# Kernel optimization log

Hardware: AMD Instinct MI355X
Metric: run time of the kernel (lower is better)

The kernel has to match this reference:

```python
import jax, jax.numpy as jnp
import numpy as np

N = 50000   # nodes
D = 64      # feature_dim
E = 800000  # edges per edge set
NEG_SLOPE = 0.2  # PyG GATConv default


def gat_conv(x, edge_index, W, a_src, a_dst, bias):
    """PyG GATConv, heads=1, concat=True, add_self_loops=True.
    h = x W; e_{j->i} = leakyrelu(a_src.h_j + a_dst.h_i); segment-softmax over dst.
    """
    n = x.shape[0]
    h = x @ W                                   # [N, D]
    s = h @ a_src                               # [N] per-node src score
    d = h @ a_dst                               # [N] per-node dst score
    src, dst = edge_index[0], edge_index[1]
    e = jax.nn.leaky_relu(s[src] + d[dst], NEG_SLOPE)
    # remove_self_loops: mask any pre-existing self loops out of the softmax
    e = jnp.where(src == dst, jnp.float32(-1e9), e)
    # add_self_loops: one (i, i) edge per node
    loop = jnp.arange(n)
    src_all = jnp.concatenate([src, loop])
    dst_all = jnp.concatenate([dst, loop])
    e_all = jnp.concatenate([e, jax.nn.leaky_relu(s + d, NEG_SLOPE)])
    # numerically stable segment softmax over incoming edges of each dst node
    m = jax.ops.segment_max(e_all, dst_all, num_segments=n)
    p = jnp.exp(e_all - m[dst_all])
    denom = jax.ops.segment_sum(p, dst_all, num_segments=n)
    alpha = p / denom[dst_all]                  # [E + N]
    out = jax.ops.segment_sum(alpha[:, None] * h[src_all], dst_all, num_segments=n)
    return out + bias


def encode(x, edge_a, edge_b, W, a_src, a_dst, bias):
    # Original overwrites x_a/x_b each loop iteration, always reading the
    # original x, so only the final-layer encoder's single application survives.
    x_a = jax.nn.relu(gat_conv(x, edge_a, W, a_src, a_dst, bias))
    x_b = jax.nn.relu(gat_conv(x, edge_b, W, a_src, a_dst, bias))
    return x_a, x_b


def setup_inputs() -> dict:
    key = jax.random.key(0)
    ks = jax.random.split(key, 13)
    edges = [jax.random.randint(ks[i], (2, E), 0, N) for i in range(8)]
    x = jax.random.normal(ks[8], (N, D), dtype=jnp.float32)
    scale = np.float32(1.0 / np.sqrt(D))
    W = jax.random.normal(ks[9], (4, D, D), dtype=jnp.float32) * scale
    a_src = jax.random.normal(ks[10], (4, D), dtype=jnp.float32) * scale
    a_dst = jax.random.normal(ks[11], (4, D), dtype=jnp.float32) * scale
    bias = jnp.zeros((4, D), dtype=jnp.float32)
    return {"edge_tp_a": edges[0], "edge_tp_b": edges[1], "edge_tn_a": edges[2],
            "edge_tn_b": edges[3], "edge_dp_a": edges[4], "edge_dp_b": edges[5],
            "edge_dn_a": edges[6], "edge_dn_b": edges[7], "x": x, "W": W,
            "a_src": a_src, "a_dst": a_dst, "bias": bias}


def reference(edge_tp_a, edge_tp_b, edge_tn_a, edge_tn_b, edge_dp_a, edge_dp_b,
              edge_dn_a, edge_dn_b, x, W, a_src, a_dst, bias):
    # 4 encode calls, each with its own (fresh) GATConv parameters
    tp_a, tp_b = encode(x, edge_tp_a, edge_tp_b, W[0], a_src[0], a_dst[0], bias[0])
    tn_a, tn_b = encode(x, edge_tn_a, edge_tn_b, W[1], a_src[1], a_dst[1], bias[1])
    dp_a, dp_b = encode(x, edge_dp_a, edge_dp_b, W[2], a_src[2], a_dst[2], bias[2])
    dn_a, dn_b = encode(x, edge_dn_a, edge_dn_b, W[3], a_src[3], a_dst[3], bias[3])
    # original return order
    return (tp_a, tp_b, dp_a, dp_b, tn_a, tn_b, dn_a, dn_b)
```

## Files before the change

kernel.cpp:

```cpp
#include <hip/hip_runtime.h>
#include <hip/hip_bf16.h>

typedef unsigned int u32;
typedef unsigned short u16;
typedef __hip_bfloat16 bf16;

typedef __attribute__((ext_vector_type(8))) short short8;
typedef __attribute__((ext_vector_type(4))) float float4v;

#define CAP 5120

__device__ __forceinline__ float lrelu(float v) { return v > 0.f ? v : 0.2f * v; }

__device__ __forceinline__ u16 f2b(float f) {
  u32 x = __float_as_uint(f);
  u32 r = (x + 0x7fffu + ((x >> 16) & 1u)) >> 16;
  return (u16)r;
}
__device__ __forceinline__ float b2fbits(u16 b) {
  return __uint_as_float(((u32)b) << 16);
}
__device__ __forceinline__ float blo(u32 v) { return __uint_as_float(v << 16); }
__device__ __forceinline__ float bhi(u32 v) { return __uint_as_float(v & 0xffff0000u); }

struct EdgePtrs { const int* e[8]; };

__global__ __launch_bounds__(256) void CSGDN_32031866093637_kernel(u32* __restrict__ p,
                                                                   int count) {
  int i = blockIdx.x * 256 + threadIdx.x;
  if (i < count) p[i] = 0;
}


__device__ __forceinline__ void gemm_role(
    u32* smem, int g, const float* __restrict__ x, const float* __restrict__ W,
    const float* __restrict__ a_src, const float* __restrict__ a_dst,
    u16* __restrict__ H, float* __restrict__ sv, float* __restrict__ dv, int n) {
  const int p = g & 3;
  const int rowbase = (g >> 2) * 64;
  const int tid = threadIdx.x, lane = tid & 63, wv = tid >> 6;
  short* xl = (short*)smem;
  short* wl = xl + 64 * 72;
#pragma unroll
  for (int it = 0; it < 16; it++) {
    int idx = it * 256 + tid;
    int r = idx >> 6, c = idx & 63;
    int gr = rowbase + r; if (gr > n - 1) gr = n - 1;
    xl[r * 72 + c] = (short)f2b(x[(size_t)gr * 64 + c]);
  }
#pragma unroll
  for (int it = 0; it < 16; it++) {
    int idx = it * 256 + tid;
    int k = idx >> 6, nc = idx & 63;
    wl[nc * 72 + k] = (short)f2b(W[p * 4096 + k * 64 + nc]);
  }
  __syncthreads();

  const int q = lane >> 4, c15 = lane & 15;
  const int wrow0 = wv * 16;
  short8 af0 = *(const short8*)&xl[(wrow0 + c15) * 72 + 0 * 32 + q * 8];
  short8 af1 = *(const short8*)&xl[(wrow0 + c15) * 72 + 1 * 32 + q * 8];
  float4v acc[4];
#pragma unroll
  for (int nt = 0; nt < 4; nt++) {
    acc[nt] = (float4v){0.f, 0.f, 0.f, 0.f};
    short8 b0 = *(const short8*)&wl[(nt * 16 + c15) * 72 + 0 * 32 + q * 8];
    short8 b1 = *(const short8*)&wl[(nt * 16 + c15) * 72 + 1 * 32 + q * 8];
    acc[nt] = __builtin_amdgcn_mfma_f32_16x16x32_bf16(af0, b0, acc[nt], 0, 0, 0);
    acc[nt] = __builtin_amdgcn_mfma_f32_16x16x32_bf16(af1, b1, acc[nt], 0, 0, 0);
  }
  u16* Hb = H + (size_t)p * n * 64;
  float as4[4], ad4[4];
#pragma unroll
  for (int nt = 0; nt < 4; nt++) {
    as4[nt] = a_src[p * 64 + nt * 16 + c15];
    ad4[nt] = a_dst[p * 64 + nt * 16 + c15];
  }
#pragma unroll
  for (int r = 0; r < 4; r++) {
    int row_g = rowbase + wrow0 + q * 4 + r;
    bool ok = row_g < n;
#pragma unroll
    for (int nt = 0; nt < 4; nt++) {
      if (ok) Hb[(size_t)row_g * 64 + nt * 16 + c15] = f2b(acc[nt][r]);
    }
    float ps = 0.f, pd = 0.f;
#pragma unroll
    for (int nt = 0; nt < 4; nt++) {
      ps = fmaf(acc[nt][r], as4[nt], ps);
      pd = fmaf(acc[nt][r], ad4[nt], pd);
    }
#pragma unroll
    for (int o = 1; o < 16; o <<= 1) {
      ps += __shfl_xor(ps, o, 64);
      pd += __shfl_xor(pd, o, 64);
    }
    if (ok && c15 == 0) {
      sv[(size_t)p * n + row_g] = ps;
      dv[(size_t)p * n + row_g] = pd;
    }
  }
}

__device__ __forceinline__ void bin_role(
    u32* smem, int bf, EdgePtrs ep, u32* __restrict__ gcnt, u32* __restrict__ bbuf,
    int E, int nb) {
  int set = bf & 7, chunk = bf >> 3;
  const int* e = ep.e[set];
  u32* hist = smem;
  u32* gbase = smem + 256;
  u32* curs = smem + 512;
  u32* loffs = smem + 768;
  u32* sorted = smem + 1028;
  int tid = threadIdx.x, lane = tid & 63, wv = tid >> 6;
  hist[tid] = 0;
  curs[tid] = 0;
  __syncthreads();
  int start = chunk * 4096;
  u32 pk_r[16];
#pragma unroll
  for (int t = 0; t < 16; t++) {
    int i = start + t * 256 + tid;
    u32 pk = 0xffffffffu;
    if (i < E) {
      int s = e[i], d = e[E + i];
      if (s != d) {
        pk = ((u32)d << 16) | (u32)s;
        atomicAdd(&hist[d >> 8], 1u);
      }
    }
    pk_r[t] = pk;
  }
  __syncthreads();
  if (hist[tid] > 0) gbase[tid] = atomicAdd(&gcnt[set * nb + tid], hist[tid]);
  if (wv == 0) {
    u32 carry = 0;
    for (int base = 0; base < 256; base += 64) {
      u32 v = hist[base + lane], x = v;
#pragma unroll
      for (int o = 1; o < 64; o <<= 1) { u32 y = __shfl_up(x, o, 64); if (lane >= o) x += y; }
      loffs[base + lane] = carry + x - v;
      carry += __shfl(x, 63, 64);
    }
    if (lane == 0) loffs[256] = carry;
  }
  __syncthreads();
#pragma unroll
  for (int t = 0; t < 16; t++) {
    u32 pk = pk_r[t];
    if (pk != 0xffffffffu) {
      int b = pk >> 24;
      u32 pos = loffs[b] + atomicAdd(&curs[b], 1u);
      sorted[pos] = pk;
    }
  }
  __syncthreads();
  int cnt = (int)loffs[256];
  for (int j = tid; j < cnt; j += 256) {
    u32 pk = sorted[j];
    int b = pk >> 24;
    u32 gpos = gbase[b] + ((u32)j - loffs[b]);
    if (gpos >= CAP) gpos = CAP - 1;
    bbuf[((size_t)(set * nb + b)) * CAP + gpos] = pk;
  }
}

__global__ __launch_bounds__(256) void prep_kernel(
    EdgePtrs ep, u32* __restrict__ gcnt, u32* __restrict__ bbuf, int E, int nb,
    int nbin,
    const float* __restrict__ x, const float* __restrict__ W,
    const float* __restrict__ a_src, const float* __restrict__ a_dst,
    u16* __restrict__ H, float* __restrict__ sv, float* __restrict__ dv, int n) {
  __shared__ __align__(16) u32 smem[5248];
  int f = blockIdx.x;
  if (f < nbin) bin_role(smem, f, ep, gcnt, bbuf, E, nb);
  else gemm_role(smem, f - nbin, x, W, a_src, a_dst, H, sv, dv, n);
}

__global__ __launch_bounds__(512) void agg_kernel(
    const u32* __restrict__ gcnt, const u32* __restrict__ bbuf,
    const u16* __restrict__ H, const float* __restrict__ sv,
    const float* __restrict__ dv, const float* __restrict__ bias,
    float* __restrict__ out, int n, int nb) {
  const int omap[8] = {0, 1, 4, 5, 2, 3, 6, 7};
  int f = blockIdx.x;
  int set = f & 7, b = f >> 3, p = set >> 1;
  int tid = threadIdx.x, lane = tid & 63, wv = tid >> 6;
  int node0 = b << 8;
  int nn = min(256, n - node0);
  __shared__ u16 ss[CAP];
  __shared__ float spe[CAP];
  __shared__ u32 hist[256], offs[257], curs[256];
  __shared__ float dpw[256], spw[256];
  const float* sp = sv + (size_t)p * n;
  const float* dp = dv + (size_t)p * n;
  for (int i = tid; i < 256; i += 512) { hist[i] = 0; curs[i] = 0; }
  for (int i = tid; i < nn; i += 512) { dpw[i] = dp[node0 + i]; spw[i] = sp[node0 + i]; }
  __syncthreads();
  int cnt = (int)gcnt[set * nb + b];
  if (cnt > CAP) cnt = CAP;
  const u32* eb = bbuf + ((size_t)(set * nb + b)) * CAP;
  u32 pk_r[10];
  float pe_r[10];
#pragma unroll
  for (int t = 0; t < 10; t++) {
    int j = t * 512 + tid;
    u32 pk = 0;
    float pe = 0.f;
    if (j < cnt) {
      pk = eb[j];
      int s = pk & 0xffff, dl = (pk >> 16) & 255;
      atomicAdd(&hist[dl], 1u);
      pe = __expf(lrelu(sp[s] + dpw[dl]));
    }
    pk_r[t] = pk;
    pe_r[t] = pe;
  }
  __syncthreads();
  if (wv == 0) {
    u32 carry = 0;
    for (int base = 0; base < 256; base += 64) {
      u32 v = hist[base + lane];
      u32 x = v;
#pragma unroll
      for (int o = 1; o < 64; o <<= 1) { u32 y = __shfl_up(x, o, 64); if (lane >= o) x += y; }
      offs[base + lane] = carry + x - v;
      carry += __shfl(x, 63, 64);
    }
    if (lane == 0) offs[256] = carry;
  }
  __syncthreads();
#pragma unroll
  for (int t = 0; t < 10; t++) {
    int j = t * 512 + tid;
    if (j < cnt) {
      u32 pk = pk_r[t];
      int dl = (pk >> 16) & 255;
      u32 pos = offs[dl] + atomicAdd(&curs[dl], 1u);
      ss[pos] = (u16)(pk & 0xffff);
      spe[pos] = pe_r[t];
    }
  }
  __syncthreads();
  const u16* Hp = H + (size_t)p * n * 64;
  const int g = lane >> 3, sub = lane & 7;
  float4v bv0 = *(const float4v*)&bias[p * 64 + sub * 8];
  float4v bv1 = *(const float4v*)&bias[p * 64 + sub * 8 + 4];
  float* op = out + (size_t)omap[set] * n * 64;
  for (int r0 = 0; r0 < nn; r0 += 64) {
    int i = r0 + wv * 8 + g;
    bool valid = i < nn;
    int iv = valid ? i : 0;
    int beg = (int)offs[iv], end2 = (int)offs[iv + 1];
    int cntg = valid ? (end2 - beg) : 0;
    int node = node0 + iv;
    float pself = valid ? __expf(lrelu(spw[iv] + dpw[iv])) : 0.f;
    uint4 hs = *(const uint4*)(Hp + ((size_t)node << 6) + (sub << 3));
    float den = pself;
    float a0 = pself * blo(hs.x), a1 = pself * bhi(hs.x);
    float a2 = pself * blo(hs.y), a3 = pself * bhi(hs.y);
    float a4 = pself * blo(hs.z), a5 = pself * bhi(hs.z);
    float a6 = pself * blo(hs.w), a7 = pself * bhi(hs.w);
    int tmax = cntg;
#pragma unroll
    for (int o = 8; o < 64; o <<= 1) tmax = max(tmax, __shfl_xor(tmax, o, 64));
    for (int t = 0; t < tmax; t += 4) {
      bool c0 = t < cntg, c1 = t + 1 < cntg, c2 = t + 2 < cntg, c3 = t + 3 < cntg;
      int j0 = c0 ? beg + t : 0;
      int j1 = c1 ? beg + t + 1 : 0;
      int j2 = c2 ? beg + t + 2 : 0;
      int j3 = c3 ? beg + t + 3 : 0;
      float pe0 = c0 ? spe[j0] : 0.f;
      float pe1 = c1 ? spe[j1] : 0.f;
      float pe2 = c2 ? spe[j2] : 0.f;
      float pe3 = c3 ? spe[j3] : 0.f;
      int s0 = ss[j0], s1 = ss[j1], s2 = ss[j2], s3 = ss[j3];
      uint4 hv0 = *(const uint4*)(Hp + ((size_t)s0 << 6) + (sub << 3));
      uint4 hv1 = *(const uint4*)(Hp + ((size_t)s1 << 6) + (sub << 3));
      uint4 hv2 = *(const uint4*)(Hp + ((size_t)s2 << 6) + (sub << 3));
      uint4 hv3 = *(const uint4*)(Hp + ((size_t)s3 << 6) + (sub << 3));
      a0 = fmaf(pe0, blo(hv0.x), a0); a1 = fmaf(pe0, bhi(hv0.x), a1);
      a2 = fmaf(pe0, blo(hv0.y), a2); a3 = fmaf(pe0, bhi(hv0.y), a3);
      a4 = fmaf(pe0, blo(hv0.z), a4); a5 = fmaf(pe0, bhi(hv0.z), a5);
      a6 = fmaf(pe0, blo(hv0.w), a6); a7 = fmaf(pe0, bhi(hv0.w), a7);
      a0 = fmaf(pe1, blo(hv1.x), a0); a1 = fmaf(pe1, bhi(hv1.x), a1);
      a2 = fmaf(pe1, blo(hv1.y), a2); a3 = fmaf(pe1, bhi(hv1.y), a3);
      a4 = fmaf(pe1, blo(hv1.z), a4); a5 = fmaf(pe1, bhi(hv1.z), a5);
      a6 = fmaf(pe1, blo(hv1.w), a6); a7 = fmaf(pe1, bhi(hv1.w), a7);
      a0 = fmaf(pe2, blo(hv2.x), a0); a1 = fmaf(pe2, bhi(hv2.x), a1);
      a2 = fmaf(pe2, blo(hv2.y), a2); a3 = fmaf(pe2, bhi(hv2.y), a3);
      a4 = fmaf(pe2, blo(hv2.z), a4); a5 = fmaf(pe2, bhi(hv2.z), a5);
      a6 = fmaf(pe2, blo(hv2.w), a6); a7 = fmaf(pe2, bhi(hv2.w), a7);
      a0 = fmaf(pe3, blo(hv3.x), a0); a1 = fmaf(pe3, bhi(hv3.x), a1);
      a2 = fmaf(pe3, blo(hv3.y), a2); a3 = fmaf(pe3, bhi(hv3.y), a3);
      a4 = fmaf(pe3, blo(hv3.z), a4); a5 = fmaf(pe3, bhi(hv3.z), a5);
      a6 = fmaf(pe3, blo(hv3.w), a6); a7 = fmaf(pe3, bhi(hv3.w), a7);
      den += (pe0 + pe1) + (pe2 + pe3);
    }
    if (valid) {
      float rd = 1.f / den;
      float4v o0 = {fmaxf(fmaf(a0, rd, bv0.x), 0.f), fmaxf(fmaf(a1, rd, bv0.y), 0.f),
                    fmaxf(fmaf(a2, rd, bv0.z), 0.f), fmaxf(fmaf(a3, rd, bv0.w), 0.f)};
      float4v o1 = {fmaxf(fmaf(a4, rd, bv1.x), 0.f), fmaxf(fmaf(a5, rd, bv1.y), 0.f),
                    fmaxf(fmaf(a6, rd, bv1.z), 0.f), fmaxf(fmaf(a7, rd, bv1.w), 0.f)};
      *(float4v*)&op[((size_t)node << 6) + (sub << 3)] = o0;
      *(float4v*)&op[((size_t)node << 6) + (sub << 3) + 4] = o1;
    }
  }
}

extern "C" void kernel_launch(void* const* d_in, const int* in_sizes, int n_in,
                              void* d_out, int out_size, void* d_ws, size_t ws_size,
                              hipStream_t stream) {
  const int E = in_sizes[0] / 2;
  const int n = in_sizes[8] / 64;
  const int nb = (n + 255) >> 8;
  const float* x = (const float*)d_in[8];
  const float* W = (const float*)d_in[9];
  const float* a_src = (const float*)d_in[10];
  const float* a_dst = (const float*)d_in[11];
  const float* bias = (const float*)d_in[12];
  float* out = (float*)d_out;

  char* ws = (char*)d_ws;
  auto alloc = [&](size_t bytes) {
    char* p = ws;
    ws += (bytes + 255) & ~(size_t)255;
    return p;
  };
  u16* H = (u16*)alloc((size_t)4 * n * 64 * 2);
  float* sv = (float*)alloc((size_t)4 * n * 4);
  float* dv = (float*)alloc((size_t)4 * n * 4);
  u32* gcnt = (u32*)alloc((size_t)8 * nb * 4);
  u32* bbuf = (u32*)alloc((size_t)8 * nb * CAP * 4);

  EdgePtrs ep;
  for (int i = 0; i < 8; i++) ep.e[i] = (const int*)d_in[i];

  const int ebpb = (E + 4095) / 4096;
  const int nbin = 8 * ebpb;
  const int ngemm = ((n + 63) / 64) * 4;

  dim3 b256(256);
  CSGDN_32031866093637_kernel<<<(8 * nb + 255) / 256, b256, 0, stream>>>(gcnt, 8 * nb);
  prep_kernel<<<nbin + ngemm, b256, 0, stream>>>(ep, gcnt, bbuf, E, nb, nbin,
                                                 x, W, a_src, a_dst, H, sv, dv, n);
  agg_kernel<<<nb * 8, dim3(512), 0, stream>>>(gcnt, bbuf, H, sv, dv, bias, out, n, nb);
}
```

Baseline: 294.8 us.

## Split aggregation into sort phase and grid-synced balanced gather phase

Converts the aggregation kernel into a persistent cooperative kernel. Phase one sorts each bucket's edges in LDS and writes the sorted sources, exp scores and per-node row ranges to global memory. After a grid-wide sync, phase two gives each block an even contiguous node range per edge set and gathers from global. This removes the per-wave max-degree padding and load imbalance, at the cost of an extra global round trip of the sorted edge data and a grid barrier.

Measured after the change: 491.5 us. +66.7%, slower.

```diff
diff --git a/kernel.cpp b/kernel.cpp
--- a/kernel.cpp
+++ b/kernel.cpp
@@ -1,5 +1,8 @@
 #include <hip/hip_runtime.h>
 #include <hip/hip_bf16.h>
+#include <hip/hip_cooperative_groups.h>
+
+namespace cg = cooperative_groups;
 
 typedef unsigned int u32;
 typedef unsigned short u16;
@@ -177,134 +180,159 @@
   else gemm_role(smem, f - nbin, x, W, a_src, a_dst, H, sv, dv, n);
 }
 
-__global__ __launch_bounds__(512) void agg_kernel(
+__global__ __launch_bounds__(512, 8) void agg_fused(
     const u32* __restrict__ gcnt, const u32* __restrict__ bbuf,
     const u16* __restrict__ H, const float* __restrict__ sv,
     const float* __restrict__ dv, const float* __restrict__ bias,
-    float* __restrict__ out, int n, int nb) {
+    float* __restrict__ out, u16* __restrict__ s_srt, float* __restrict__ pe_srt,
+    u32* __restrict__ rs, u32* __restrict__ rc, int n, int nb) {
   const int omap[8] = {0, 1, 4, 5, 2, 3, 6, 7};
-  int f = blockIdx.x;
-  int set = f & 7, b = f >> 3, p = set >> 1;
-  int tid = threadIdx.x, lane = tid & 63, wv = tid >> 6;
-  int node0 = b << 8;
-  int nn = min(256, n - node0);
+  const int tid = threadIdx.x, lane = tid & 63, wv = tid >> 6;
   __shared__ u16 ss[CAP];
   __shared__ float spe[CAP];
   __shared__ u32 hist[256], offs[257], curs[256];
-  __shared__ float dpw[256], spw[256];
-  const float* sp = sv + (size_t)p * n;
-  const float* dp = dv + (size_t)p * n;
-  for (int i = tid; i < 256; i += 512) { hist[i] = 0; curs[i] = 0; }
-  for (int i = tid; i < nn; i += 512) { dpw[i] = dp[node0 + i]; spw[i] = sp[node0 + i]; }
-  __syncthreads();
-  int cnt = (int)gcnt[set * nb + b];
-  if (cnt > CAP) cnt = CAP;
-  const u32* eb = bbuf + ((size_t)(set * nb + b)) * CAP;
-  u32 pk_r[10];
-  float pe_r[10];
-#pragma unroll
-  for (int t = 0; t < 10; t++) {
-    int j = t * 512 + tid;
-    u32 pk = 0;
-    float pe = 0.f;
-    if (j < cnt) {
-      pk = eb[j];
-      int s = pk & 0xffff, dl = (pk >> 16) & 255;
-      atomicAdd(&hist[dl], 1u);
-      pe = __expf(lrelu(sp[s] + dpw[dl]));
-    }
-    pk_r[t] = pk;
-    pe_r[t] = pe;
-  }
-  __syncthreads();
-  if (wv == 0) {
-    u32 carry = 0;
-    for (int base = 0; base < 256; base += 64) {
-      u32 v = hist[base + lane];
-      u32 x = v;
-#pragma unroll
-      for (int o = 1; o < 64; o <<= 1) { u32 y = __shfl_up(x, o, 64); if (lane >= o) x += y; }
-      offs[base + lane] = carry + x - v;
-      carry += __shfl(x, 63, 64);
-    }
-    if (lane == 0) offs[256] = carry;
-  }
-  __syncthreads();
-#pragma unroll
-  for (int t = 0; t < 10; t++) {
-    int j = t * 512 + tid;
-    if (j < cnt) {
-      u32 pk = pk_r[t];
-      int dl = (pk >> 16) & 255;
-      u32 pos = offs[dl] + atomicAdd(&curs[dl], 1u);
-      ss[pos] = (u16)(pk & 0xffff);
-      spe[pos] = pe_r[t];
-    }
-  }
-  __syncthreads();
-  const u16* Hp = H + (size_t)p * n * 64;
-  const int g = lane >> 3, sub = lane & 7;
-  float4v bv0 = *(const float4v*)&bias[p * 64 + sub * 8];
-  float4v bv1 = *(const float4v*)&bias[p * 64 + sub * 8 + 4];
-  float* op = out + (size_t)omap[set] * n * 64;
-  for (int r0 = 0; r0 < nn; r0 += 64) {
-    int i = r0 + wv * 8 + g;
-    bool valid = i < nn;
-    int iv = valid ? i : 0;
-    int beg = (int)offs[iv], end2 = (int)offs[iv + 1];
-    int cntg = valid ? (end2 - beg) : 0;
-    int node = node0 + iv;
-    float pself = valid ? __expf(lrelu(spw[iv] + dpw[iv])) : 0.f;
-    uint4 hs = *(const uint4*)(Hp + ((size_t)node << 6) + (sub << 3));
-    float den = pself;
-    float a0 = pself * blo(hs.x), a1 = pself * bhi(hs.x);
-    float a2 = pself * blo(hs.y), a3 = pself * bhi(hs.y);
-    float a4 = pself * blo(hs.z), a5 = pself * bhi(hs.z);
-    float a6 = pself * blo(hs.w), a7 = pself * bhi(hs.w);
-    int tmax = cntg;
-#pragma unroll
-    for (int o = 8; o < 64; o <<= 1) tmax = max(tmax, __shfl_xor(tmax, o, 64));
-    for (int t = 0; t < tmax; t += 4) {
-      bool c0 = t < cntg, c1 = t + 1 < cntg, c2 = t + 2 < cntg, c3 = t + 3 < cntg;
-      int j0 = c0 ? beg + t : 0;
-      int j1 = c1 ? beg + t + 1 : 0;
-      int j2 = c2 ? beg + t + 2 : 0;
-      int j3 = c3 ? beg + t + 3 : 0;
-      float pe0 = c0 ? spe[j0] : 0.f;
-      float pe1 = c1 ? spe[j1] : 0.f;
-      float pe2 = c2 ? spe[j2] : 0.f;
-      float pe3 = c3 ? spe[j3] : 0.f;
-      int s0 = ss[j0], s1 = ss[j1], s2 = ss[j2], s3 = ss[j3];
-      uint4 hv0 = *(const uint4*)(Hp + ((size_t)s0 << 6) + (sub << 3));
-      uint4 hv1 = *(const uint4*)(Hp + ((size_t)s1 << 6) + (sub << 3));
-      uint4 hv2 = *(const uint4*)(Hp + ((size_t)s2 << 6) + (sub << 3));
-      uint4 hv3 = *(const uint4*)(Hp + ((size_t)s3 << 6) + (sub << 3));
-      a0 = fmaf(pe0, blo(hv0.x), a0); a1 = fmaf(pe0, bhi(hv0.x), a1);
-      a2 = fmaf(pe0, blo(hv0.y), a2); a3 = fmaf(pe0, bhi(hv0.y), a3);
-      a4 = fmaf(pe0, blo(hv0.z), a4); a5 = fmaf(pe0, bhi(hv0.z), a5);
-      a6 = fmaf(pe0, blo(hv0.w), a6); a7 = fmaf(pe0, bhi(hv0.w), a7);
-      a0 = fmaf(pe1, blo(hv1.x), a0); a1 = fmaf(pe1, bhi(hv1.x), a1);
-      a2 = fmaf(pe1, blo(hv1.y), a2); a3 = fmaf(pe1, bhi(hv1.y), a3);
-      a4 = fmaf(pe1, blo(hv1.z), a4); a5 = fmaf(pe1, bhi(hv1.z), a5);
-      a6 = fmaf(pe1, blo(hv1.w), a6); a7 = fmaf(pe1, bhi(hv1.w), a7);
-      a0 = fmaf(pe2, blo(hv2.x), a0); a1 = fmaf(pe2, bhi(hv2.x), a1);
-      a2 = fmaf(pe2, blo(hv2.y), a2); a3 = fmaf(pe2, bhi(hv2.y), a3);
-      a4 = fmaf(pe2, blo(hv2.z), a4); a5 = fmaf(pe2, bhi(hv2.z), a5);
-      a6 = fmaf(pe2, blo(hv2.w), a6); a7 = fmaf(pe2, bhi(hv2.w), a7);
-      a0 = fmaf(pe3, blo(hv3.x), a0); a1 = fmaf(pe3, bhi(hv3.x), a1);
-      a2 = fmaf(pe3, blo(hv3.y), a2); a3 = fmaf(pe3, bhi(hv3.y), a3);
-      a4 = fmaf(pe3, blo(hv3.z), a4); a5 = fmaf(pe3, bhi(hv3.z), a5);
-      a6 = fmaf(pe3, blo(hv3.w), a6); a7 = fmaf(pe3, bhi(hv3.w), a7);
-      den += (pe0 + pe1) + (pe2 + pe3);
-    }
-    if (valid) {
-      float rd = 1.f / den;
-      float4v o0 = {fmaxf(fmaf(a0, rd, bv0.x), 0.f), fmaxf(fmaf(a1, rd, bv0.y), 0.f),
-                    fmaxf(fmaf(a2, rd, bv0.z), 0.f), fmaxf(fmaf(a3, rd, bv0.w), 0.f)};
-      float4v o1 = {fmaxf(fmaf(a4, rd, bv1.x), 0.f), fmaxf(fmaf(a5, rd, bv1.y), 0.f),
-                    fmaxf(fmaf(a6, rd, bv1.z), 0.f), fmaxf(fmaf(a7, rd, bv1.w), 0.f)};
-      *(float4v*)&op[((size_t)node << 6) + (sub << 3)] = o0;
-      *(float4v*)&op[((size_t)node << 6) + (sub << 3) + 4] = o1;
+  __shared__ float dpw[256];
+
+  const int ntask = 8 * nb;
+  for (int task = blockIdx.x; task < ntask; task += gridDim.x) {
+    int set = task & 7, b = task >> 3, p = set >> 1;
+    int node0 = b << 8;
+    int nn = min(256, n - node0);
+    const float* sp = sv + (size_t)p * n;
+    const float* dp = dv + (size_t)p * n;
+    for (int i = tid; i < 256; i += 512) { hist[i] = 0; curs[i] = 0; }
+    for (int i = tid; i < nn; i += 512) dpw[i] = dp[node0 + i];
+    __syncthreads();
+    int cnt = (int)gcnt[set * nb + b];
+    if (cnt > CAP) cnt = CAP;
+    size_t ebase = (size_t)(set * nb + b) * CAP;
+    const u32* eb = bbuf + ebase;
+    u32 pk_r[10];
+    float pe_r[10];
+#pragma unroll
+    for (int t = 0; t < 10; t++) {
+      int j = t * 512 + tid;
+      u32 pk = 0;
+      float pe = 0.f;
+      if (j < cnt) {
+        pk = eb[j];
+        int s = pk & 0xffff, dl = (pk >> 16) & 255;
+        atomicAdd(&hist[dl], 1u);
+        pe = __expf(lrelu(sp[s] + dpw[dl]));
+      }
+      pk_r[t] = pk;
+      pe_r[t] = pe;
+    }
+    __syncthreads();
+    if (wv == 0) {
+      u32 carry = 0;
+      for (int base = 0; base < 256; base += 64) {
+        u32 v = hist[base + lane];
+        u32 x = v;
+#pragma unroll
+        for (int o = 1; o < 64; o <<= 1) { u32 y = __shfl_up(x, o, 64); if (lane >= o) x += y; }
+        offs[base + lane] = carry + x - v;
+        carry += __shfl(x, 63, 64);
+      }
+      if (lane == 0) offs[256] = carry;
+    }
+    __syncthreads();
+#pragma unroll
+    for (int t = 0; t < 10; t++) {
+      int j = t * 512 + tid;
+      if (j < cnt) {
+        u32 pk = pk_r[t];
+        int dl = (pk >> 16) & 255;
+        u32 pos = offs[dl] + atomicAdd(&curs[dl], 1u);
+        ss[pos] = (u16)(pk & 0xffff);
+        spe[pos] = pe_r[t];
+      }
+    }
+    __syncthreads();
+    for (int j = tid; j < cnt; j += 512) {
+      s_srt[ebase + j] = ss[j];
+      pe_srt[ebase + j] = spe[j];
+    }
+    for (int i = tid; i < nn; i += 512) {
+      rs[(size_t)set * n + node0 + i] = (u32)ebase + offs[i];
+      rc[(size_t)set * n + node0 + i] = offs[i + 1] - offs[i];
+    }
+    __syncthreads();
+  }
+
+  __threadfence();
+  cg::this_grid().sync();
+
+  {
+    int set = blockIdx.x & 7, p = set >> 1;
+    int bps = gridDim.x >> 3;
+    int blk = blockIdx.x >> 3;
+    int nch = (n + bps - 1) / bps;
+    int lo = blk * nch, hi = min(n, lo + nch);
+    const int g = lane >> 3, sub = lane & 7;
+    const u16* Hp = H + (size_t)p * n * 64;
+    const float* sp = sv + (size_t)p * n;
+    const float* dp = dv + (size_t)p * n;
+    const u32* rsp = rs + (size_t)set * n;
+    const u32* rcp = rc + (size_t)set * n;
+    float4v bv0 = *(const float4v*)&bias[p * 64 + sub * 8];
+    float4v bv1 = *(const float4v*)&bias[p * 64 + sub * 8 + 4];
+    float* op = out + (size_t)omap[set] * n * 64;
+    for (int base = lo; base < hi; base += 64) {
+      int node = base + wv * 8 + g;
+      bool valid = node < hi;
+      int nd = valid ? node : lo;
+      int beg = (int)rsp[nd];
+      int cntg = valid ? (int)rcp[nd] : 0;
+      float pself = valid ? __expf(lrelu(sp[nd] + dp[nd])) : 0.f;
+      uint4 hs = *(const uint4*)(Hp + ((size_t)nd << 6) + (sub << 3));
+      float den = pself;
+      float a0 = pself * blo(hs.x), a1 = pself * bhi(hs.x);
+      float a2 = pself * blo(hs.y), a3 = pself * bhi(hs.y);
+      float a4 = pself * blo(hs.z), a5 = pself * bhi(hs.z);
+      float a6 = pself * blo(hs.w), a7 = pself * bhi(hs.w);
+      for (int t = 0; t < cntg; t += 4) {
+        bool c1 = t + 1 < cntg, c2 = t + 2 < cntg, c3 = t + 3 < cntg;
+        int j0 = beg + t;
+        int j1 = c1 ? j0 + 1 : j0;
+        int j2 = c2 ? j0 + 2 : j0;
+        int j3 = c3 ? j0 + 3 : j0;
+        float pe0 = pe_srt[j0];
+        float pe1 = pe_srt[j1]; if (!c1) pe1 = 0.f;
+        float pe2 = pe_srt[j2]; if (!c2) pe2 = 0.f;
+        float pe3 = pe_srt[j3]; if (!c3) pe3 = 0.f;
+        int s0 = s_srt[j0], s1 = s_srt[j1], s2 = s_srt[j2], s3 = s_srt[j3];
+        uint4 hv0 = *(const uint4*)(Hp + ((size_t)s0 << 6) + (sub << 3));
+        uint4 hv1 = *(const uint4*)(Hp + ((size_t)s1 << 6) + (sub << 3));
+        uint4 hv2 = *(const uint4*)(Hp + ((size_t)s2 << 6) + (sub << 3));
+        uint4 hv3 = *(const uint4*)(Hp + ((size_t)s3 << 6) + (sub << 3));
+        a0 = fmaf(pe0, blo(hv0.x), a0); a1 = fmaf(pe0, bhi(hv0.x), a1);
+        a2 = fmaf(pe0, blo(hv0.y), a2); a3 = fmaf(pe0, bhi(hv0.y), a3);
+        a4 = fmaf(pe0, blo(hv0.z), a4); a5 = fmaf(pe0, bhi(hv0.z), a5);
+        a6 = fmaf(pe0, blo(hv0.w), a6); a7 = fmaf(pe0, bhi(hv0.w), a7);
+        a0 = fmaf(pe1, blo(hv1.x), a0); a1 = fmaf(pe1, bhi(hv1.x), a1);
+        a2 = fmaf(pe1, blo(hv1.y), a2); a3 = fmaf(pe1, bhi(hv1.y), a3);
+        a4 = fmaf(pe1, blo(hv1.z), a4); a5 = fmaf(pe1, bhi(hv1.z), a5);
+        a6 = fmaf(pe1, blo(hv1.w), a6); a7 = fmaf(pe1, bhi(hv1.w), a7);
+        a0 = fmaf(pe2, blo(hv2.x), a0); a1 = fmaf(pe2, bhi(hv2.x), a1);
+        a2 = fmaf(pe2, blo(hv2.y), a2); a3 = fmaf(pe2, bhi(hv2.y), a3);
+        a4 = fmaf(pe2, blo(hv2.z), a4); a5 = fmaf(pe2, bhi(hv2.z), a5);
+        a6 = fmaf(pe2, blo(hv2.w), a6); a7 = fmaf(pe2, bhi(hv2.w), a7);
+        a0 = fmaf(pe3, blo(hv3.x), a0); a1 = fmaf(pe3, bhi(hv3.x), a1);
+        a2 = fmaf(pe3, blo(hv3.y), a2); a3 = fmaf(pe3, bhi(hv3.y), a3);
+        a4 = fmaf(pe3, blo(hv3.z), a4); a5 = fmaf(pe3, bhi(hv3.z), a5);
+        a6 = fmaf(pe3, blo(hv3.w), a6); a7 = fmaf(pe3, bhi(hv3.w), a7);
+        den += (pe0 + pe1) + (pe2 + pe3);
+      }
+      if (valid) {
+        float rd = 1.f / den;
+        float4v o0 = {fmaxf(fmaf(a0, rd, bv0.x), 0.f), fmaxf(fmaf(a1, rd, bv0.y), 0.f),
+                      fmaxf(fmaf(a2, rd, bv0.z), 0.f), fmaxf(fmaf(a3, rd, bv0.w), 0.f)};
+        float4v o1 = {fmaxf(fmaf(a4, rd, bv1.x), 0.f), fmaxf(fmaf(a5, rd, bv1.y), 0.f),
+                      fmaxf(fmaf(a6, rd, bv1.z), 0.f), fmaxf(fmaf(a7, rd, bv1.w), 0.f)};
+        *(float4v*)&op[((size_t)nd << 6) + (sub << 3)] = o0;
+        *(float4v*)&op[((size_t)nd << 6) + (sub << 3) + 4] = o1;
+      }
     }
   }
 }
@@ -333,6 +361,10 @@
   float* dv = (float*)alloc((size_t)4 * n * 4);
   u32* gcnt = (u32*)alloc((size_t)8 * nb * 4);
   u32* bbuf = (u32*)alloc((size_t)8 * nb * CAP * 4);
+  u16* s_srt = (u16*)alloc((size_t)8 * nb * CAP * 2);
+  float* pe_srt = (float*)alloc((size_t)8 * nb * CAP * 4);
+  u32* rs = (u32*)alloc((size_t)8 * n * 4);
+  u32* rc = (u32*)alloc((size_t)8 * n * 4);
 
   EdgePtrs ep;
   for (int i = 0; i < 8; i++) ep.e[i] = (const int*)d_in[i];
@@ -345,5 +377,15 @@
   CSGDN_32031866093637_kernel<<<(8 * nb + 255) / 256, b256, 0, stream>>>(gcnt, 8 * nb);
   prep_kernel<<<nbin + ngemm, b256, 0, stream>>>(ep, gcnt, bbuf, E, nb, nbin,
                                                  x, W, a_src, a_dst, H, sv, dv, n);
-  agg_kernel<<<nb * 8, dim3(512), 0, stream>>>(gcnt, bbuf, H, sv, dv, bias, out, n, nb);
-}
+
+  int maxb = 0;
+  hipOccupancyMaxActiveBlocksPerMultiprocessor(&maxb, agg_fused, 512, 0);
+  if (maxb < 1) maxb = 1;
+  int grid = (maxb * 256) & ~7;
+  if (grid < 8) grid = 8;
+  int n_loc = n, nb_loc = nb;
+  void* kargs[] = {(void*)&gcnt, (void*)&bbuf, (void*)&H, (void*)&sv, (void*)&dv,
+                   (void*)&bias, (void*)&out, (void*)&s_srt, (void*)&pe_srt,
+                   (void*)&rs, (void*)&rc, (void*)&n_loc, (void*)&nb_loc};
+  hipLaunchCooperativeKernel(agg_fused, dim3(grid), dim3(512), kargs, 0, stream);
+}
```
